# Optimization experiments

Hardware: AMD Instinct MI355X
Metric: run time of the kernel (lower is better)

## Reference

```python
import jax, jax.numpy as jnp
import numpy as np

N, E, H = 50000, 800000, 4
IN_C, HID, OUT = 256, 64, 64
NEG_SLOPE = 0.2   # PyG GATConv default leaky_relu slope
EPS_BN = 1e-5
EPS_SM = 1e-16    # PyG softmax denominator eps


def setup_inputs() -> dict:
    key = jax.random.key(0)
    ks = jax.random.split(key, 16)
    inp = {
        "x": jax.random.normal(ks[0], (N, IN_C), jnp.float32),
        "edge_index": jax.random.randint(ks[1], (2, E), 0, N, jnp.int32),
    }
    dims = [(IN_C, HID), (HID, HID), (HID, OUT)]
    j = 2
    for l, (di, do) in enumerate(dims):
        s = 1.0 / np.sqrt(di)
        inp[f"W{l}"] = jax.random.normal(ks[j], (di, H * do), jnp.float32) * s; j += 1
        inp[f"as{l}"] = jax.random.normal(ks[j], (H, do), jnp.float32) * 0.1; j += 1
        inp[f"ad{l}"] = jax.random.normal(ks[j], (H, do), jnp.float32) * 0.1; j += 1
        inp[f"b{l}"] = jnp.zeros((do,), jnp.float32)
    for l in range(2):  # BN after all but the last conv
        inp[f"g{l}"] = jnp.ones((HID,), jnp.float32)
        inp[f"be{l}"] = jnp.zeros((HID,), jnp.float32)
    return inp


def _gat_layer(x, src, dst, W, a_src, a_dst, bias):
    """PyG GATConv, heads=H, concat=False (mean over heads), add_self_loops already in src/dst."""
    n = x.shape[0]
    C = a_src.shape[1]
    h = (x @ W).reshape(n, H, C)                      # [N,H,C]
    a_l = jnp.einsum('nhc,hc->nh', h, a_src)          # src attention term per node
    a_r = jnp.einsum('nhc,hc->nh', h, a_dst)          # dst attention term per node
    e = jax.nn.leaky_relu(a_l[src] + a_r[dst], NEG_SLOPE)   # [E',H]
    # segment softmax over incoming edges of each dst node
    m = jax.ops.segment_max(e, dst, num_segments=n)
    m = jnp.where(jnp.isfinite(m), m, 0.0)
    p = jnp.exp(e - m[dst])
    den = jax.ops.segment_sum(p, dst, num_segments=n)
    alpha = p / (den[dst] + EPS_SM)                   # [E',H]
    msg = h[src] * alpha[:, :, None]                  # [E',H,C]
    out = jax.ops.segment_sum(msg, dst, num_segments=n)
    return out.mean(axis=1) + bias                    # concat=False -> head mean, then bias


def _bn(x, g, b):
    # BatchNorm1d training-mode statistics (biased variance), eps=1e-5
    mu = x.mean(axis=0)
    var = x.var(axis=0)
    return (x - mu) * jax.lax.rsqrt(var + EPS_BN) * g + b


def reference(x, edge_index, W0, as0, ad0, b0, W1, as1, ad1, b1,
              W2, as2, ad2, b2, g0, be0, g1, be1):
    n = x.shape[0]
    loops = jnp.arange(n, dtype=edge_index.dtype)
    src = jnp.concatenate([edge_index[0], loops])
    dst = jnp.concatenate([edge_index[1], loops])

    h = _gat_layer(x, src, dst, W0, as0, ad0, b0)
    h = jax.nn.relu(_bn(h, g0, be0))                  # dropout: eval mode (identity)
    h = _gat_layer(h, src, dst, W1, as1, ad1, b1)
    h = jax.nn.relu(_bn(h, g1, be1))
    out = _gat_layer(h, src, dst, W2, as2, ad2, b2)
    return out
```

## Files before the change

### kernel.cpp

```cpp
#include <hip/hip_runtime.h>
#include <hip/hip_fp16.h>
#include <math.h>

constexpr float NEG_SLOPE = 0.2f;
constexpr float EPS_BN = 1e-5f;
constexpr float EPS_SM = 1e-16f;

typedef _Float16 half8 __attribute__((ext_vector_type(8)));
typedef float f32x4 __attribute__((ext_vector_type(4)));

__device__ __forceinline__ float lrelu(float x){ return x >= 0.f ? x : NEG_SLOPE * x; }

__global__ void k_prep(int* cnt, int n, float* bn, int* tick,
                       const float* __restrict__ W0, const float* __restrict__ W1,
                       const float* __restrict__ W2, _Float16* __restrict__ Wt0,
                       _Float16* __restrict__ Wt1, _Float16* __restrict__ Wt2){
  int t = blockIdx.x * blockDim.x + threadIdx.x;
  if (t < n) cnt[t] = 1;
  if (t < 256) bn[t] = 0.f;
  if (t < 4) tick[t] = 0;
  if (t < 65536){
    int c = t & 255, k = t >> 8;
    Wt0[(size_t)c * 256 + k] = (_Float16)W0[(size_t)k * 256 + c];
  } else if (t < 81920){
    int u = t - 65536; int c = u & 255, k = u >> 8;
    Wt1[(size_t)c * 64 + k] = (_Float16)W1[(size_t)k * 256 + c];
  } else if (t < 98304){
    int u = t - 81920; int c = u & 255, k = u >> 8;
    Wt2[(size_t)c * 64 + k] = (_Float16)W2[(size_t)k * 256 + c];
  }
}

__global__ void k_count(const int* __restrict__ ei, int E, int* __restrict__ cnt){
  int e = blockIdx.x * blockDim.x + threadIdx.x;
  if (e >= E) return;
  atomicAdd(&cnt[ei[E + e]], 1);
}

__global__ __launch_bounds__(256) void k_bsumscan(const int* __restrict__ cnt, int n, int chunk,
                                                  int* __restrict__ part, int* __restrict__ ptr,
                                                  int* __restrict__ tick){
  __shared__ int s[256];
  __shared__ int amLast;
  int b = blockIdx.x, t = threadIdx.x;
  int lo = b * chunk, hi = min(n, lo + chunk);
  int v = 0;
  for (int i = lo + t; i < hi; i += 256) v += cnt[i];
  s[t] = v;
  __syncthreads();
  #pragma unroll
  for (int off = 128; off > 0; off >>= 1){
    if (t < off) s[t] += s[t + off];
    __syncthreads();
  }
  if (t == 0) part[b] = s[0];
  __threadfence();
  if (t == 0) amLast = (atomicAdd(tick, 1) == (int)gridDim.x - 1) ? 1 : 0;
  __syncthreads();
  if (amLast){
    int pv = atomicAdd(&part[t], 0);
    s[t] = pv;
    __syncthreads();
    #pragma unroll
    for (int off = 1; off < 256; off <<= 1){
      int u = (t >= off) ? s[t - off] : 0;
      __syncthreads();
      s[t] += u;
      __syncthreads();
    }
    part[t] = s[t] - pv;
    if (t == 255) ptr[n] = s[255];
  }
}

__global__ __launch_bounds__(256) void k_localscan(const int* __restrict__ cnt, const int* __restrict__ part,
                                                   int n, int chunk, int* __restrict__ ptr,
                                                   int* __restrict__ cursor, int* __restrict__ csr_src){
  __shared__ int s[256];
  int b = blockIdx.x, t = threadIdx.x;
  int i = b * chunk + t;
  int v = (t < chunk && i < n) ? cnt[i] : 0;
  s[t] = v;
  __syncthreads();
  #pragma unroll
  for (int off = 1; off < 256; off <<= 1){
    int u = (t >= off) ? s[t - off] : 0;
    __syncthreads();
    s[t] += u;
    __syncthreads();
  }
  if (t < chunk && i < n){
    int ex = part[b] + s[t] - v;
    ptr[i] = ex;
    cursor[i] = ex;
    csr_src[ex + v - 1] = i;
  }
}

__global__ void k_fill(const int* __restrict__ ei, int E,
                       int* __restrict__ cursor, int* __restrict__ csr_src){
  int e = blockIdx.x * blockDim.x + threadIdx.x;
  if (e >= E) return;
  int src = ei[e], dst = ei[E + e];
  int slot = atomicAdd(&cursor[dst], 1);
  csr_src[slot] = src;
}

__global__ __launch_bounds__(256, 2) void k_gemm(const float* __restrict__ X,
    const _Float16* __restrict__ Wt, const float* __restrict__ a_s, const float* __restrict__ a_d,
    __half* __restrict__ hb, float* __restrict__ al, float* __restrict__ ar, int nrows, int K,
    const float* __restrict__ scale, const float* __restrict__ shift){
  __shared__ _Float16 Alds[4][129][8];
  __shared__ _Float16 Blds[4][257][8];
  int tid = threadIdx.x;
  int m0 = blockIdx.x * 128;
  int w = tid >> 6, l = tid & 63;
  int lm = l & 15, lq = l >> 4;
  int qs = tid & 3, rs = tid >> 2;
  f32x4 acc[8][4] = {};

  for (int k0 = 0; k0 < K; k0 += 32){
    float4 sc0, sc1, sh0, sh1;
    if (scale){
      sc0 = *(const float4*)(scale + k0 + qs * 8);
      sc1 = *(const float4*)(scale + k0 + qs * 8 + 4);
      sh0 = *(const float4*)(shift + k0 + qs * 8);
      sh1 = *(const float4*)(shift + k0 + qs * 8 + 4);
    }
    #pragma unroll
    for (int it = 0; it < 2; it++){
      int row = it * 64 + rs;
      int gr = m0 + row;
      float4 v0 = make_float4(0,0,0,0), v1 = make_float4(0,0,0,0);
      if (gr < nrows){
        v0 = *(const float4*)(X + (size_t)gr * K + k0 + qs * 8);
        v1 = *(const float4*)(X + (size_t)gr * K + k0 + qs * 8 + 4);
      }
      if (scale){
        v0.x = fmaxf(fmaf(v0.x, sc0.x, sh0.x), 0.f);
        v0.y = fmaxf(fmaf(v0.y, sc0.y, sh0.y), 0.f);
        v0.z = fmaxf(fmaf(v0.z, sc0.z, sh0.z), 0.f);
        v0.w = fmaxf(fmaf(v0.w, sc0.w, sh0.w), 0.f);
        v1.x = fmaxf(fmaf(v1.x, sc1.x, sh1.x), 0.f);
        v1.y = fmaxf(fmaf(v1.y, sc1.y, sh1.y), 0.f);
        v1.z = fmaxf(fmaf(v1.z, sc1.z, sh1.z), 0.f);
        v1.w = fmaxf(fmaf(v1.w, sc1.w, sh1.w), 0.f);
      }
      half8 h = {(_Float16)v0.x, (_Float16)v0.y, (_Float16)v0.z, (_Float16)v0.w,
                 (_Float16)v1.x, (_Float16)v1.y, (_Float16)v1.z, (_Float16)v1.w};
      *(half8*)&Alds[qs][row][0] = h;
    }
    #pragma unroll
    for (int it = 0; it < 4; it++){
      int col = it * 64 + rs;
      *(half8*)&Blds[qs][col][0] = *(const half8*)(Wt + (size_t)col * K + k0 + qs * 8);
    }
    __syncthreads();
    half8 af[8];
    #pragma unroll
    for (int mf = 0; mf < 8; mf++) af[mf] = *(const half8*)&Alds[lq][mf * 16 + lm][0];
    #pragma unroll
    for (int j = 0; j < 4; j++){
      half8 bf = *(const half8*)&Blds[lq][(w * 4 + j) * 16 + lm][0];
      #pragma unroll
      for (int mf = 0; mf < 8; mf++)
        acc[mf][j] = __builtin_amdgcn_mfma_f32_16x16x32_f16(af[mf], bf, acc[mf][j], 0, 0, 0);
    }
    __syncthreads();
  }

  float asv[4], adv[4];
  #pragma unroll
  for (int j = 0; j < 4; j++){
    asv[j] = a_s[w * 64 + j * 16 + lm];
    adv[j] = a_d[w * 64 + j * 16 + lm];
  }
  #pragma unroll
  for (int mf = 0; mf < 8; mf++){
    #pragma unroll
    for (int reg = 0; reg < 4; reg++){
      float sl = acc[mf][0][reg] * asv[0] + acc[mf][1][reg] * asv[1]
               + acc[mf][2][reg] * asv[2] + acc[mf][3][reg] * asv[3];
      float sr = acc[mf][0][reg] * adv[0] + acc[mf][1][reg] * adv[1]
               + acc[mf][2][reg] * adv[2] + acc[mf][3][reg] * adv[3];
      #pragma unroll
      for (int off = 1; off < 16; off <<= 1){
        sl += __shfl_xor(sl, off);
        sr += __shfl_xor(sr, off);
      }
      int row = m0 + mf * 16 + lq * 4 + reg;
      if (lm == 0 && row < nrows){
        al[(size_t)row * 4 + w] = sl;
        ar[(size_t)row * 4 + w] = sr;
      }
    }
    #pragma unroll
    for (int j = 0; j < 4; j++){
      #pragma unroll
      for (int reg = 0; reg < 4; reg++){
        int row = m0 + mf * 16 + lq * 4 + reg;
        if (row < nrows)
          hb[(size_t)row * 256 + w * 64 + j * 16 + lm] = __float2half(acc[mf][j][reg]);
      }
    }
  }
}

__global__ __launch_bounds__(256) void k_node(const int* __restrict__ ptr,
    const int* __restrict__ csr, const __half* __restrict__ hb,
    const float* __restrict__ al, const float* __restrict__ ar,
    const float* __restrict__ bias, float* __restrict__ out, int N){
  __shared__ float4 wsm[4][64];
  __shared__ int    ssm[4][64];
  int n = (blockIdx.x * blockDim.x + threadIdx.x) >> 6;
  int lane = threadIdx.x & 63;
  int wv = threadIdx.x >> 6;
  if (n >= N) return;
  int beg = ptr[n], end = ptr[n + 1];
  int deg = end - beg;
  float4 arv = *(const float4*)(ar + (size_t)n * 4);

  if (deg <= 64){
    int idx = beg + lane;
    bool act = idx < end;
    int mye = act ? csr[idx] : 0;
    float e0 = -1e30f, e1 = -1e30f, e2 = -1e30f, e3 = -1e30f;
    if (act){
      float4 av = *(const float4*)((const char*)al + ((unsigned)mye << 4));
      e0 = lrelu(av.x + arv.x); e1 = lrelu(av.y + arv.y);
      e2 = lrelu(av.z + arv.z); e3 = lrelu(av.w + arv.w);
    }
    float m0 = e0, m1 = e1, m2 = e2, m3 = e3;
    #pragma unroll
    for (int off = 32; off > 0; off >>= 1){
      m0 = fmaxf(m0, __shfl_xor(m0, off));
      m1 = fmaxf(m1, __shfl_xor(m1, off));
      m2 = fmaxf(m2, __shfl_xor(m2, off));
      m3 = fmaxf(m3, __shfl_xor(m3, off));
    }
    float w0 = __expf(e0 - m0), w1 = __expf(e1 - m1);
    float w2 = __expf(e2 - m2), w3 = __expf(e3 - m3);
    float d0 = w0, d1 = w1, d2 = w2, d3 = w3;
    #pragma unroll
    for (int off = 32; off > 0; off >>= 1){
      d0 += __shfl_xor(d0, off);
      d1 += __shfl_xor(d1, off);
      d2 += __shfl_xor(d2, off);
      d3 += __shfl_xor(d3, off);
    }
    wsm[wv][lane] = make_float4(w0 / (d0 + EPS_SM), w1 / (d1 + EPS_SM),
                                w2 / (d2 + EPS_SM), w3 / (d3 + EPS_SM));
    ssm[wv][lane] = mye;
    __builtin_amdgcn_wave_barrier();

    int eh = lane >> 5;
    int hd = (lane >> 3) & 3;
    int c8 = lane & 7;
    unsigned choff = (unsigned)(hd * 128 + c8 * 16);
    const float* wbase = (const float*)&wsm[wv][0];
    float a0=0.f,a1=0.f,a2=0.f,a3=0.f,a4=0.f,a5=0.f,a6=0.f,a7=0.f;
    #pragma unroll 2
    for (int j = 0; j < deg; j += 2){
      int je = j + eh;
      int s = ssm[wv][je];
      float w = wbase[je * 4 + hd];
      int4 q = *(const int4*)((const char*)hb + (((unsigned)s << 9) + choff));
      const __half2* h2 = (const __half2*)&q;
      float2 f0 = __half22float2(h2[0]);
      float2 f1 = __half22float2(h2[1]);
      float2 f2 = __half22float2(h2[2]);
      float2 f3 = __half22float2(h2[3]);
      a0 = fmaf(f0.x, w, a0); a1 = fmaf(f0.y, w, a1);
      a2 = fmaf(f1.x, w, a2); a3 = fmaf(f1.y, w, a3);
      a4 = fmaf(f2.x, w, a4); a5 = fmaf(f2.y, w, a5);
      a6 = fmaf(f3.x, w, a6); a7 = fmaf(f3.y, w, a7);
    }
    #pragma unroll
    for (int off = 32; off >= 8; off >>= 1){
      a0 += __shfl_xor(a0, off); a1 += __shfl_xor(a1, off);
      a2 += __shfl_xor(a2, off); a3 += __shfl_xor(a3, off);
      a4 += __shfl_xor(a4, off); a5 += __shfl_xor(a5, off);
      a6 += __shfl_xor(a6, off); a7 += __shfl_xor(a7, off);
    }
    if (lane < 8){
      float* op = out + (size_t)n * 64 + c8 * 8;
      float4 b0 = *(const float4*)(bias + c8 * 8);
      float4 b1 = *(const float4*)(bias + c8 * 8 + 4);
      *(float4*)op       = make_float4(a0*0.25f+b0.x, a1*0.25f+b0.y, a2*0.25f+b0.z, a3*0.25f+b0.w);
      *(float4*)(op + 4) = make_float4(a4*0.25f+b1.x, a5*0.25f+b1.y, a6*0.25f+b1.z, a7*0.25f+b1.w);
    }
  } else {
    int hd = lane >> 4;
    int cg = (lane & 15) * 4;
    const __half* hbase = hb + hd * 64 + cg;
    float ax = 0.f, ay = 0.f, az = 0.f, aw = 0.f;
    float m0 = -1e30f, m1 = -1e30f, m2 = -1e30f, m3 = -1e30f;
    for (int i = beg + lane; i < end; i += 64){
      int s = csr[i];
      float4 av = *(const float4*)(al + (size_t)s * 4);
      m0 = fmaxf(m0, lrelu(av.x + arv.x));
      m1 = fmaxf(m1, lrelu(av.y + arv.y));
      m2 = fmaxf(m2, lrelu(av.z + arv.z));
      m3 = fmaxf(m3, lrelu(av.w + arv.w));
    }
    #pragma unroll
    for (int off = 32; off > 0; off >>= 1){
      m0 = fmaxf(m0, __shfl_xor(m0, off));
      m1 = fmaxf(m1, __shfl_xor(m1, off));
      m2 = fmaxf(m2, __shfl_xor(m2, off));
      m3 = fmaxf(m3, __shfl_xor(m3, off));
    }
    float d0 = 0.f, d1 = 0.f, d2 = 0.f, d3 = 0.f;
    for (int i = beg + lane; i < end; i += 64){
      int s = csr[i];
      float4 av = *(const float4*)(al + (size_t)s * 4);
      d0 += __expf(lrelu(av.x + arv.x) - m0);
      d1 += __expf(lrelu(av.y + arv.y) - m1);
      d2 += __expf(lrelu(av.z + arv.z) - m2);
      d3 += __expf(lrelu(av.w + arv.w) - m3);
    }
    #pragma unroll
    for (int off = 32; off > 0; off >>= 1){
      d0 += __shfl_xor(d0, off);
      d1 += __shfl_xor(d1, off);
      d2 += __shfl_xor(d2, off);
      d3 += __shfl_xor(d3, off);
    }
    float i0 = 1.f / (d0 + EPS_SM), i1 = 1.f / (d1 + EPS_SM);
    float i2 = 1.f / (d2 + EPS_SM), i3 = 1.f / (d3 + EPS_SM);
    float arh = hd == 0 ? arv.x : hd == 1 ? arv.y : hd == 2 ? arv.z : arv.w;
    float mh  = hd == 0 ? m0 : hd == 1 ? m1 : hd == 2 ? m2 : m3;
    float ih  = hd == 0 ? i0 : hd == 1 ? i1 : hd == 2 ? i2 : i3;
    for (int i = beg; i < end; i++){
      int s = csr[i];
      float w = __expf(lrelu(al[(size_t)s * 4 + hd] + arh) - mh) * ih;
      ushort4 u = *(const ushort4*)(hbase + (size_t)s * 256);
      ax = fmaf(__half2float(__ushort_as_half(u.x)), w, ax);
      ay = fmaf(__half2float(__ushort_as_half(u.y)), w, ay);
      az = fmaf(__half2float(__ushort_as_half(u.z)), w, az);
      aw = fmaf(__half2float(__ushort_as_half(u.w)), w, aw);
    }
    #pragma unroll
    for (int off = 16; off <= 32; off <<= 1){
      ax += __shfl_xor(ax, off);
      ay += __shfl_xor(ay, off);
      az += __shfl_xor(az, off);
      aw += __shfl_xor(aw, off);
    }
    if (lane < 16){
      float4 b4 = *(const float4*)(bias + cg);
      *(float4*)(out + (size_t)n * 64 + cg) =
          make_float4(ax * 0.25f + b4.x, ay * 0.25f + b4.y, az * 0.25f + b4.z, aw * 0.25f + b4.w);
    }
  }
}

__global__ __launch_bounds__(256) void k_bnstats(const float* __restrict__ x, int N,
                                                 float* __restrict__ gsum, float* __restrict__ gsq,
                                                 int* __restrict__ tick,
                                                 const float* __restrict__ g, const float* __restrict__ be,
                                                 float* __restrict__ scale, float* __restrict__ shift){
  int c = threadIdx.x & 63;
  int rg = threadIdx.x >> 6;
  float s = 0.f, q = 0.f;
  for (int r = blockIdx.x * 4 + rg; r < N; r += gridDim.x * 4){
    float v = x[(size_t)r * 64 + c];
    s += v; q += v * v;
  }
  __shared__ float ls[4][64], lq[4][64];
  __shared__ int amLast;
  ls[rg][c] = s; lq[rg][c] = q;
  __syncthreads();
  if (rg == 0){
    s = ls[0][c] + ls[1][c] + ls[2][c] + ls[3][c];
    q = lq[0][c] + lq[1][c] + lq[2][c] + lq[3][c];
    atomicAdd(&gsum[c], s);
    atomicAdd(&gsq[c], q);
  }
  __threadfence();
  if (threadIdx.x == 0)
    amLast = (atomicAdd(tick, 1) == (int)gridDim.x - 1) ? 1 : 0;
  __syncthreads();
  if (amLast && threadIdx.x < 64){
    float gs = atomicAdd(&gsum[c], 0.f);
    float gq = atomicAdd(&gsq[c], 0.f);
    float m = gs / (float)N;
    float v = gq / (float)N - m * m;
    float sc = g[c] * rsqrtf(v + EPS_BN);
    scale[c] = sc;
    shift[c] = be[c] - m * sc;
  }
}

extern "C" void kernel_launch(void* const* d_in, const int* in_sizes, int n_in,
                              void* d_out, int out_size, void* d_ws, size_t ws_size,
                              hipStream_t stream){
  const float* x  = (const float*)d_in[0];
  const int*   ei = (const int*)d_in[1];
  const float* W[3]  = {(const float*)d_in[2], (const float*)d_in[6],  (const float*)d_in[10]};
  const float* AS[3] = {(const float*)d_in[3], (const float*)d_in[7],  (const float*)d_in[11]};
  const float* AD[3] = {(const float*)d_in[4], (const float*)d_in[8],  (const float*)d_in[12]};
  const float* BI[3] = {(const float*)d_in[5], (const float*)d_in[9],  (const float*)d_in[13]};
  const float* G[2]  = {(const float*)d_in[14], (const float*)d_in[16]};
  const float* BE[2] = {(const float*)d_in[15], (const float*)d_in[17]};
  const int N = in_sizes[0] / 256;
  const int E = in_sizes[1] / 2;
  const int EN = E + N;

  char* wsb = (char*)d_ws;
  size_t off = 0;
  auto alloc = [&](size_t bytes) -> char* {
    char* p = wsb + off;
    off = (off + bytes + 255) & ~(size_t)255;
    return p;
  };
  int* cnt      = (int*)alloc((size_t)N * 4);
  int* cursor   = (int*)alloc((size_t)N * 4);
  int* rowptr   = (int*)alloc((size_t)(N + 1) * 4);
  int* part     = (int*)alloc(256 * 4);
  int* csr      = (int*)alloc((size_t)EN * 4);
  _Float16* Wt0 = (_Float16*)alloc((size_t)256 * 256 * 2);
  _Float16* Wt1 = (_Float16*)alloc((size_t)64 * 256 * 2);
  _Float16* Wt2 = (_Float16*)alloc((size_t)64 * 256 * 2);
  __half* hb    = (__half*)alloc((size_t)N * 256 * 2);
  float* al     = (float*)alloc((size_t)N * 4 * 4);
  float* ar     = (float*)alloc((size_t)N * 4 * 4);
  float* bufA   = (float*)alloc((size_t)N * 64 * 4);
  float* bn     = (float*)alloc(256 * 4);
  int*   tick   = (int*)alloc(4 * 4);
  float* murs   = (float*)alloc(128 * 4);

  const int chunk = (N + 255) / 256;

  k_prep<<<384, 256, 0, stream>>>(cnt, N, bn, tick, W[0], W[1], W[2], Wt0, Wt1, Wt2);
  k_count<<<(E + 255) / 256, 256, 0, stream>>>(ei, E, cnt);
  k_bsumscan<<<256, 256, 0, stream>>>(cnt, N, chunk, part, rowptr, tick + 2);
  k_localscan<<<256, 256, 0, stream>>>(cnt, part, N, chunk, rowptr, cursor, csr);
  k_fill<<<(E + 255) / 256, 256, 0, stream>>>(ei, E, cursor, csr);

  const _Float16* Wt[3] = {Wt0, Wt1, Wt2};
  const float* lin = x;
  for (int l = 0; l < 3; l++){
    int K = (l == 0) ? 256 : 64;
    const float* sc = (l == 0) ? nullptr : murs;
    const float* sh = (l == 0) ? nullptr : murs + 64;
    k_gemm<<<(N + 127) / 128, 256, 0, stream>>>(lin, Wt[l], AS[l], AD[l], hb, al, ar, N, K, sc, sh);
    float* outp = (l == 2) ? (float*)d_out : bufA;
    k_node<<<(N + 3) / 4, 256, 0, stream>>>(rowptr, csr, hb, al, ar, BI[l], outp, N);
    if (l < 2){
      float* gsum = bn + l * 128;
      float* gsq  = gsum + 64;
      k_bnstats<<<128, 256, 0, stream>>>(bufA, N, gsum, gsq, tick + l, G[l], BE[l], murs, murs + 64);
      lin = bufA;
    }
  }
}
```

Baseline: 565.8 us.

## Pre-convert x to fp16, use direct global-to-LDS loads in GEMM, fuse count into prep

Adds a prep kernel that converts x to fp16 in one pass and also does the destination-degree atomic counting, which removes the separate count kernel. The GEMM is templated per layer with K fixed at compile time. Layer 0 A tiles and all W tiles are now loaded with global_load_lds, which writes straight into LDS without going through registers. This aims to halve the A-tile read traffic in the layer-0 GEMM and cut register and VALU pressure, but it adds an extra full pass over x (read fp32, write fp16) and an extra buffer.

```diff
diff --git a/kernel.cpp b/kernel.cpp
--- a/kernel.cpp
+++ b/kernel.cpp
@@ -11,14 +11,34 @@
 
 __device__ __forceinline__ float lrelu(float x){ return x >= 0.f ? x : NEG_SLOPE * x; }
 
-__global__ void k_prep(int* cnt, int n, float* bn, int* tick,
-                       const float* __restrict__ W0, const float* __restrict__ W1,
-                       const float* __restrict__ W2, _Float16* __restrict__ Wt0,
-                       _Float16* __restrict__ Wt1, _Float16* __restrict__ Wt2){
+typedef const __attribute__((address_space(1))) unsigned int* gas_u32;
+typedef __attribute__((address_space(3))) unsigned int* las_u32;
+
+__device__ __forceinline__ void llds16(const _Float16* g, _Float16* l){
+  __builtin_amdgcn_global_load_lds((gas_u32)(const void*)g, (las_u32)(void*)l, 16, 0, 0);
+}
+
+__global__ void k_prep0(int* cnt, int n, float* bn, int* tick){
   int t = blockIdx.x * blockDim.x + threadIdx.x;
   if (t < n) cnt[t] = 1;
   if (t < 256) bn[t] = 0.f;
   if (t < 4) tick[t] = 0;
+}
+
+__global__ void k_prep1(const float* __restrict__ x, _Float16* __restrict__ xh, int n8,
+                        const int* __restrict__ ei, int E, int* __restrict__ cnt,
+                        const float* __restrict__ W0, const float* __restrict__ W1,
+                        const float* __restrict__ W2, _Float16* __restrict__ Wt0,
+                        _Float16* __restrict__ Wt1, _Float16* __restrict__ Wt2){
+  int t = blockIdx.x * blockDim.x + threadIdx.x;
+  if (t < n8){
+    const float4* p = (const float4*)(x + (size_t)t * 8);
+    float4 v0 = p[0], v1 = p[1];
+    half8 h = {(_Float16)v0.x, (_Float16)v0.y, (_Float16)v0.z, (_Float16)v0.w,
+               (_Float16)v1.x, (_Float16)v1.y, (_Float16)v1.z, (_Float16)v1.w};
+    *(half8*)(xh + (size_t)t * 8) = h;
+  }
+  if (t < E) atomicAdd(&cnt[ei[E + t]], 1);
   if (t < 65536){
     int c = t & 255, k = t >> 8;
     Wt0[(size_t)c * 256 + k] = (_Float16)W0[(size_t)k * 256 + c];
@@ -29,12 +49,6 @@
     int u = t - 81920; int c = u & 255, k = u >> 8;
     Wt2[(size_t)c * 64 + k] = (_Float16)W2[(size_t)k * 256 + c];
   }
-}
-
-__global__ void k_count(const int* __restrict__ ei, int E, int* __restrict__ cnt){
-  int e = blockIdx.x * blockDim.x + threadIdx.x;
-  if (e >= E) return;
-  atomicAdd(&cnt[ei[E + e]], 1);
 }
 
 __global__ __launch_bounds__(256) void k_bsumscan(const int* __restrict__ cnt, int n, int chunk,
@@ -106,37 +120,43 @@
   csr_src[slot] = src;
 }
 
-__global__ __launch_bounds__(256, 2) void k_gemm(const float* __restrict__ X,
+template<int LAYER>
+__global__ __launch_bounds__(256, 2) void k_gemm(const _Float16* __restrict__ Xh,
+    const float* __restrict__ Xf,
     const _Float16* __restrict__ Wt, const float* __restrict__ a_s, const float* __restrict__ a_d,
-    __half* __restrict__ hb, float* __restrict__ al, float* __restrict__ ar, int nrows, int K,
+    __half* __restrict__ hb, float* __restrict__ al, float* __restrict__ ar, int nrows,
     const float* __restrict__ scale, const float* __restrict__ shift){
+  constexpr int K = (LAYER == 0) ? 256 : 64;
   __shared__ _Float16 Alds[4][129][8];
   __shared__ _Float16 Blds[4][257][8];
   int tid = threadIdx.x;
   int m0 = blockIdx.x * 128;
   int w = tid >> 6, l = tid & 63;
   int lm = l & 15, lq = l >> 4;
-  int qs = tid & 3, rs = tid >> 2;
   f32x4 acc[8][4] = {};
 
   for (int k0 = 0; k0 < K; k0 += 32){
-    float4 sc0, sc1, sh0, sh1;
-    if (scale){
-      sc0 = *(const float4*)(scale + k0 + qs * 8);
-      sc1 = *(const float4*)(scale + k0 + qs * 8 + 4);
-      sh0 = *(const float4*)(shift + k0 + qs * 8);
-      sh1 = *(const float4*)(shift + k0 + qs * 8 + 4);
-    }
-    #pragma unroll
-    for (int it = 0; it < 2; it++){
-      int row = it * 64 + rs;
-      int gr = m0 + row;
-      float4 v0 = make_float4(0,0,0,0), v1 = make_float4(0,0,0,0);
-      if (gr < nrows){
-        v0 = *(const float4*)(X + (size_t)gr * K + k0 + qs * 8);
-        v1 = *(const float4*)(X + (size_t)gr * K + k0 + qs * 8 + 4);
+    if (LAYER == 0){
+      #pragma unroll
+      for (int it = 0; it < 2; it++){
+        int gr = m0 + it * 64 + l;
+        if (gr < nrows)
+          llds16(Xh + (size_t)gr * K + k0 + w * 8, &Alds[w][it * 64][0]);
       }
-      if (scale){
+    } else {
+      float4 sc0 = *(const float4*)(scale + k0 + w * 8);
+      float4 sc1 = *(const float4*)(scale + k0 + w * 8 + 4);
+      float4 sh0 = *(const float4*)(shift + k0 + w * 8);
+      float4 sh1 = *(const float4*)(shift + k0 + w * 8 + 4);
+      #pragma unroll
+      for (int it = 0; it < 2; it++){
+        int row = it * 64 + l;
+        int gr = m0 + row;
+        float4 v0 = make_float4(0,0,0,0), v1 = make_float4(0,0,0,0);
+        if (gr < nrows){
+          v0 = *(const float4*)(Xf + (size_t)gr * K + k0 + w * 8);
+          v1 = *(const float4*)(Xf + (size_t)gr * K + k0 + w * 8 + 4);
+        }
         v0.x = fmaxf(fmaf(v0.x, sc0.x, sh0.x), 0.f);
         v0.y = fmaxf(fmaf(v0.y, sc0.y, sh0.y), 0.f);
         v0.z = fmaxf(fmaf(v0.z, sc0.z, sh0.z), 0.f);
@@ -145,15 +165,15 @@
         v1.y = fmaxf(fmaf(v1.y, sc1.y, sh1.y), 0.f);
         v1.z = fmaxf(fmaf(v1.z, sc1.z, sh1.z), 0.f);
         v1.w = fmaxf(fmaf(v1.w, sc1.w, sh1.w), 0.f);
+        half8 h = {(_Float16)v0.x, (_Float16)v0.y, (_Float16)v0.z, (_Float16)v0.w,
+                   (_Float16)v1.x, (_Float16)v1.y, (_Float16)v1.z, (_Float16)v1.w};
+        *(half8*)&Alds[w][row][0] = h;
       }
-      half8 h = {(_Float16)v0.x, (_Float16)v0.y, (_Float16)v0.z, (_Float16)v0.w,
-                 (_Float16)v1.x, (_Float16)v1.y, (_Float16)v1.z, (_Float16)v1.w};
-      *(half8*)&Alds[qs][row][0] = h;
     }
     #pragma unroll
     for (int it = 0; it < 4; it++){
-      int col = it * 64 + rs;
-      *(half8*)&Blds[qs][col][0] = *(const half8*)(Wt + (size_t)col * K + k0 + qs * 8);
+      int col = it * 64 + l;
+      llds16(Wt + (size_t)col * K + k0 + w * 8, &Blds[w][it * 64][0]);
     }
     __syncthreads();
     half8 af[8];
@@ -419,6 +439,7 @@
   int* rowptr   = (int*)alloc((size_t)(N + 1) * 4);
   int* part     = (int*)alloc(256 * 4);
   int* csr      = (int*)alloc((size_t)EN * 4);
+  _Float16* xh  = (_Float16*)alloc((size_t)N * 256 * 2);
   _Float16* Wt0 = (_Float16*)alloc((size_t)256 * 256 * 2);
   _Float16* Wt1 = (_Float16*)alloc((size_t)64 * 256 * 2);
   _Float16* Wt2 = (_Float16*)alloc((size_t)64 * 256 * 2);
@@ -431,27 +452,25 @@
   float* murs   = (float*)alloc(128 * 4);
 
   const int chunk = (N + 255) / 256;
-
-  k_prep<<<384, 256, 0, stream>>>(cnt, N, bn, tick, W[0], W[1], W[2], Wt0, Wt1, Wt2);
-  k_count<<<(E + 255) / 256, 256, 0, stream>>>(ei, E, cnt);
+  const int n8 = N * 32;
+
+  k_prep0<<<(N + 255) / 256, 256, 0, stream>>>(cnt, N, bn, tick);
+  k_prep1<<<(n8 + 255) / 256, 256, 0, stream>>>(x, xh, n8, ei, E, cnt,
+                                                W[0], W[1], W[2], Wt0, Wt1, Wt2);
   k_bsumscan<<<256, 256, 0, stream>>>(cnt, N, chunk, part, rowptr, tick + 2);
   k_localscan<<<256, 256, 0, stream>>>(cnt, part, N, chunk, rowptr, cursor, csr);
   k_fill<<<(E + 255) / 256, 256, 0, stream>>>(ei, E, cursor, csr);
 
-  const _Float16* Wt[3] = {Wt0, Wt1, Wt2};
-  const float* lin = x;
-  for (int l = 0; l < 3; l++){
-    int K = (l == 0) ? 256 : 64;
-    const float* sc = (l == 0) ? nullptr : murs;
-    const float* sh = (l == 0) ? nullptr : murs + 64;
-    k_gemm<<<(N + 127) / 128, 256, 0, stream>>>(lin, Wt[l], AS[l], AD[l], hb, al, ar, N, K, sc, sh);
-    float* outp = (l == 2) ? (float*)d_out : bufA;
-    k_node<<<(N + 3) / 4, 256, 0, stream>>>(rowptr, csr, hb, al, ar, BI[l], outp, N);
-    if (l < 2){
-      float* gsum = bn + l * 128;
-      float* gsq  = gsum + 64;
-      k_bnstats<<<128, 256, 0, stream>>>(bufA, N, gsum, gsq, tick + l, G[l], BE[l], murs, murs + 64);
-      lin = bufA;
-    }
-  }
-}
+  int gemmGrid = (N + 127) / 128;
+  k_gemm<0><<<gemmGrid, 256, 0, stream>>>(xh, nullptr, Wt0, AS[0], AD[0], hb, al, ar, N,
+                                          nullptr, nullptr);
+  k_node<<<(N + 3) / 4, 256, 0, stream>>>(rowptr, csr, hb, al, ar, BI[0], bufA, N);
+  k_bnstats<<<128, 256, 0, stream>>>(bufA, N, bn, bn + 64, tick, G[0], BE[0], murs, murs + 64);
+  k_gemm<1><<<gemmGrid, 256, 0, stream>>>(nullptr, bufA, Wt1, AS[1], AD[1], hb, al, ar, N,
+                                          murs, murs + 64);
+  k_node<<<(N + 3) / 4, 256, 0, stream>>>(rowptr, csr, hb, al, ar, BI[1], bufA, N);
+  k_bnstats<<<128, 256, 0, stream>>>(bufA, N, bn + 128, bn + 192, tick + 1, G[1], BE[1], murs, murs + 64);
+  k_gemm<2><<<gemmGrid, 256, 0, stream>>>(nullptr, bufA, Wt2, AS[2], AD[2], hb, al, ar, N,
+                                          murs, murs + 64);
+  k_node<<<(N + 3) / 4, 256, 0, stream>>>(rowptr, csr, hb, al, ar, BI[2], (float*)d_out, N);
+}
```

After: 558.8 us. No clear change (-1.2%).
